# Performance work log

Measured on AMD Instinct MI355X. Metric: run time of the kernel, lower is better.

## Reference

```python
import jax, jax.numpy as jnp
import numpy as np

DIM = 768
HEADS = 6
HD = DIM // HEADS
B, N = 8, 4096
EPS = 1e-12  # torch F.normalize default


def setup_inputs() -> dict:
    key = jax.random.key(0)
    k1, k2, k3, k4, k5 = jax.random.split(key, 5)
    x = jax.random.normal(k1, (B, N, DIM), dtype=jnp.float32)
    y = jax.random.normal(k2, (B, N, DIM), dtype=jnp.float32)
    W_qkv = jax.random.normal(k3, (DIM, 2 * DIM), dtype=jnp.float32) * (1.0 / np.sqrt(DIM))
    temperature = jnp.ones((HEADS, 1, 1), dtype=jnp.float32)
    W_proj = jax.random.normal(k4, (DIM, DIM), dtype=jnp.float32) * (1.0 / np.sqrt(DIM))
    b_proj = jax.random.normal(k5, (DIM,), dtype=jnp.float32) * 0.01
    return {"x": x, "y": y, "W_qkv": W_qkv, "temperature": temperature,
            "W_proj": W_proj, "b_proj": b_proj}


def _l2norm(t):
    # F.normalize(dim=-1): v / max(||v||, eps)
    n = jnp.sqrt(jnp.sum(t * t, axis=-1, keepdims=True))
    return t / jnp.maximum(n, EPS)


def reference(x, y, W_qkv, temperature, W_proj, b_proj):
    Bx, Nx, C = x.shape
    # qkv: [B,N,2C] -> [B,N,2,H,hd] -> q,k: [B,H,hd,N]
    qkv = (x @ W_qkv).reshape(Bx, Nx, 2, HEADS, HD)
    qkv = jnp.transpose(qkv, (2, 0, 3, 4, 1))  # [2,B,H,hd,N]
    q, k = qkv[0], qkv[1]
    # v: [B,H,hd,N]
    v = jnp.transpose(y.reshape(Bx, Nx, HEADS, HD), (0, 2, 3, 1))
    q = _l2norm(q)  # normalize over token dim N
    k = _l2norm(k)
    # channel-channel attention: [B,H,hd,hd]
    attn = jnp.einsum('bhcn,bhdn->bhcd', q, k) * temperature
    attn = jax.nn.softmax(attn, axis=-1)
    out = jnp.einsum('bhcd,bhdn->bhcn', attn, v)  # [B,H,hd,N]
    out = jnp.transpose(out, (0, 3, 1, 2)).reshape(Bx, Nx, C)
    return out @ W_proj + b_proj
```

## Files before the change

### kernel.cpp

```cpp
#include <hip/hip_runtime.h>
#include <hip/hip_bf16.h>

using bf16 = __hip_bfloat16;
typedef __attribute__((ext_vector_type(4))) float f32x4;
typedef __attribute__((ext_vector_type(8))) short bf16x8;

constexpr int Ntok   = 4096;
constexpr int Cdim   = 768;
constexpr int Hn     = 6;
constexpr int HD     = 128;
constexpr int QKcols = 1536;
constexpr int NTRI   = 21;
constexpr int SPLITK = 4;

#define AS1 __attribute__((address_space(1)))
#define AS3 __attribute__((address_space(3)))

__device__ inline void gload_lds16(const bf16* g, bf16* l) {
    __builtin_amdgcn_global_load_lds((const AS1 void*)g, (AS3 void*)l, 16, 0, 0);
}

__device__ inline int4 cvt8_f32_to_bf16(const float* p) {
    const float4 a0 = *reinterpret_cast<const float4*>(p);
    const float4 a1 = *reinterpret_cast<const float4*>(p + 4);
    union { int4 i; bf16 h[8]; } u;
    u.h[0] = __float2bfloat16(a0.x); u.h[1] = __float2bfloat16(a0.y);
    u.h[2] = __float2bfloat16(a0.z); u.h[3] = __float2bfloat16(a0.w);
    u.h[4] = __float2bfloat16(a1.x); u.h[5] = __float2bfloat16(a1.y);
    u.h[6] = __float2bfloat16(a1.z); u.h[7] = __float2bfloat16(a1.w);
    return u.i;
}

__global__ __launch_bounds__(256) void cvt_kernel(const float* __restrict__ in,
                                                  bf16* __restrict__ out) {
    const size_t i = ((size_t)blockIdx.x * 256 + threadIdx.x) * 8;
    *reinterpret_cast<int4*>(out + i) = cvt8_f32_to_bf16(in + i);
}

__global__ void transpose_kernel(const float* __restrict__ W, bf16* __restrict__ Wt,
                                 int K, int N) {
    __shared__ bf16 tile[32][33];
    const int n0 = blockIdx.x * 32, k0 = blockIdx.y * 32;
    const int tx = threadIdx.x, ty = threadIdx.y;
    for (int i = 0; i < 32; i += 8)
        tile[ty + i][tx] = __float2bfloat16(W[(size_t)(k0 + ty + i) * N + n0 + tx]);
    __syncthreads();
    for (int i = 0; i < 32; i += 8)
        Wt[(size_t)(n0 + ty + i) * K + k0 + tx] = tile[tx][ty + i];
}

__global__ __launch_bounds__(256) void transpose_x(const float* __restrict__ x,
                                                   bf16* __restrict__ xT) {
    __shared__ bf16 tile[64][34];
    const int b = blockIdx.z, n0 = blockIdx.y * 64, c0 = blockIdx.x * 32;
    const int tid = threadIdx.x;
    const int c_r = tid & 31, n_r = tid >> 5;
    const float* xp = x + ((size_t)b * Ntok + n0) * Cdim + c0;
#pragma unroll
    for (int i = 0; i < 64; i += 8)
        tile[n_r + i][c_r] = __float2bfloat16(xp[(size_t)(n_r + i) * Cdim + c_r]);
    __syncthreads();
    const int n_w = tid & 63, c_w = tid >> 6;
    bf16* op = xT + ((size_t)b * Cdim + c0) * Ntok + n0;
#pragma unroll
    for (int i = 0; i < 32; i += 4)
        op[(size_t)(c_w + i) * Ntok + n_w] = tile[n_w][c_w + i];
}

template <bool C_F32, bool BIAS>
__global__ __launch_bounds__(256) void gemm_bt(const bf16* __restrict__ A,
                                               const bf16* __restrict__ Bt,
                                               const float* __restrict__ bias,
                                               void* __restrict__ Cv,
                                               int N, int K,
                                               size_t a_bs, size_t bt_bs, size_t c_bs) {
    __shared__ bf16 As[128 * 32];
    __shared__ bf16 Bs[128 * 32];

    A  += (size_t)blockIdx.z * a_bs;
    Bt += (size_t)blockIdx.z * bt_bs;
    const int m0   = blockIdx.y * 128, n0 = blockIdx.x * 128;
    const int tid  = threadIdx.x;
    const int wave = tid >> 6, lane = tid & 63;
    const int wq   = wave >> 1, wr = wave & 1;
    const int lm   = lane & 15, quad = lane >> 4;

    const int srow = tid >> 2, scol = (tid & 3) * 8;
    const bf16* Ag = A  + (size_t)(m0 + srow) * K + scol;
    const bf16* Bg = Bt + (size_t)(n0 + srow) * K + scol;
    bf16* Al0 = &As[srow * 32 + scol];
    bf16* Al1 = &As[(64 + srow) * 32 + scol];
    bf16* Bl0 = &Bs[srow * 32 + scol];
    bf16* Bl1 = &Bs[(64 + srow) * 32 + scol];

    f32x4 acc[4][4] = {};

    for (int k0 = 0; k0 < K; k0 += 32) {
        __syncthreads();
        gload_lds16(Ag + k0,                  Al0);
        gload_lds16(Ag + (size_t)64 * K + k0, Al1);
        gload_lds16(Bg + k0,                  Bl0);
        gload_lds16(Bg + (size_t)64 * K + k0, Bl1);
        __syncthreads();

        bf16x8 af[4], bfr[4];
#pragma unroll
        for (int t = 0; t < 4; t++) {
            af[t]  = *reinterpret_cast<const bf16x8*>(&As[(wq * 64 + t * 16 + lm) * 32 + quad * 8]);
            bfr[t] = *reinterpret_cast<const bf16x8*>(&Bs[(wr * 64 + t * 16 + lm) * 32 + quad * 8]);
        }
#pragma unroll
        for (int mt = 0; mt < 4; mt++)
#pragma unroll
            for (int nt = 0; nt < 4; nt++)
                acc[mt][nt] = __builtin_amdgcn_mfma_f32_16x16x32_bf16(af[mt], bfr[nt], acc[mt][nt], 0, 0, 0);
    }

    const int cm = m0 + wq * 64, cn = n0 + wr * 64;
#pragma unroll
    for (int mt = 0; mt < 4; mt++) {
#pragma unroll
        for (int nt = 0; nt < 4; nt++) {
            const int col = cn + nt * 16 + lm;
            const float bv = BIAS ? bias[col] : 0.0f;
#pragma unroll
            for (int r = 0; r < 4; r++) {
                const int row = cm + mt * 16 + quad * 4 + r;
                if constexpr (C_F32)
                    ((float*)Cv + (size_t)blockIdx.z * c_bs)[(size_t)row * N + col] = acc[mt][nt][r] + bv;
                else
                    ((bf16*)Cv + (size_t)blockIdx.z * c_bs)[(size_t)row * N + col] = __float2bfloat16(acc[mt][nt][r] + bv);
            }
        }
    }
}

__global__ __launch_bounds__(256) void gram_k(const bf16* __restrict__ xT,
                                              float* __restrict__ partial) {
    __shared__ bf16 As[128 * 32];
    __shared__ bf16 Bs[128 * 32];

    int ci = 0, rem = blockIdx.x, rowlen = 6;
    while (rem >= rowlen) { rem -= rowlen; rowlen--; ci++; }
    const int di = ci + rem;
    const int b = blockIdx.y, s = blockIdx.z;
    const int c0 = ci * 128, d0 = di * 128;

    const int tid  = threadIdx.x;
    const int wave = tid >> 6, lane = tid & 63;
    const int wq   = wave >> 1, wr = wave & 1;
    const int lm   = lane & 15, quad = lane >> 4;

    const int srow = tid >> 2, scol = (tid & 3) * 8;
    const size_t base = (size_t)b * Cdim * Ntok + (size_t)s * (Ntok / SPLITK);
    const bf16* Ag = xT + base + (size_t)(c0 + srow) * Ntok + scol;
    const bf16* Bg = xT + base + (size_t)(d0 + srow) * Ntok + scol;
    bf16* Al0 = &As[srow * 32 + scol];
    bf16* Al1 = &As[(64 + srow) * 32 + scol];
    bf16* Bl0 = &Bs[srow * 32 + scol];
    bf16* Bl1 = &Bs[(64 + srow) * 32 + scol];

    f32x4 acc[4][4] = {};

    for (int k0 = 0; k0 < Ntok / SPLITK; k0 += 32) {
        __syncthreads();
        gload_lds16(Ag + k0,                     Al0);
        gload_lds16(Ag + (size_t)64 * Ntok + k0, Al1);
        gload_lds16(Bg + k0,                     Bl0);
        gload_lds16(Bg + (size_t)64 * Ntok + k0, Bl1);
        __syncthreads();

        bf16x8 af[4], bfr[4];
#pragma unroll
        for (int t = 0; t < 4; t++) {
            af[t]  = *reinterpret_cast<const bf16x8*>(&As[(wq * 64 + t * 16 + lm) * 32 + quad * 8]);
            bfr[t] = *reinterpret_cast<const bf16x8*>(&Bs[(wr * 64 + t * 16 + lm) * 32 + quad * 8]);
        }
#pragma unroll
        for (int mt = 0; mt < 4; mt++)
#pragma unroll
            for (int nt = 0; nt < 4; nt++)
                acc[mt][nt] = __builtin_amdgcn_mfma_f32_16x16x32_bf16(af[mt], bfr[nt], acc[mt][nt], 0, 0, 0);
    }

    float* pp = partial + (((size_t)blockIdx.x * 8 + b) * SPLITK + s) * 16384;
#pragma unroll
    for (int mt = 0; mt < 4; mt++)
#pragma unroll
        for (int nt = 0; nt < 4; nt++)
#pragma unroll
            for (int r = 0; r < 4; r++)
                pp[(size_t)(wq * 64 + mt * 16 + quad * 4 + r) * 128 + wr * 64 + nt * 16 + lm] = acc[mt][nt][r];
}

__global__ __launch_bounds__(256) void gram_reduce(const float* __restrict__ partial,
                                                   bf16* __restrict__ G) {
    int ci = 0, rem = blockIdx.x, rowlen = 6;
    while (rem >= rowlen) { rem -= rowlen; rowlen--; ci++; }
    const int di = ci + rem, b = blockIdx.y;
    const int c0 = ci * 128, d0 = di * 128;
    const float* p0 = partial + ((size_t)blockIdx.x * 8 + b) * SPLITK * 16384;
    bf16* Gb = G + (size_t)b * Cdim * Cdim;
    const int tid = threadIdx.x;

    for (int i = 0; i < 16; i++) {
        const int off = i * 1024 + tid * 4;
        float4 v = *reinterpret_cast<const float4*>(p0 + off);
#pragma unroll
        for (int s2 = 1; s2 < SPLITK; s2++) {
            const float4 u = *reinterpret_cast<const float4*>(p0 + (size_t)s2 * 16384 + off);
            v.x += u.x; v.y += u.y; v.z += u.z; v.w += u.w;
        }
        const int c = off >> 7, d = off & 127;
        union { uint2 u2; bf16 h[4]; } pk;
        pk.h[0] = __float2bfloat16(v.x); pk.h[1] = __float2bfloat16(v.y);
        pk.h[2] = __float2bfloat16(v.z); pk.h[3] = __float2bfloat16(v.w);
        *reinterpret_cast<uint2*>(&Gb[(size_t)(c0 + c) * Cdim + d0 + d]) = pk.u2;
        if (ci != di) {
#pragma unroll
            for (int jj = 0; jj < 4; jj++)
                Gb[(size_t)(d0 + d + jj) * Cdim + c0 + c] = pk.h[jj];
        }
    }
}

__global__ __launch_bounds__(256) void diag_kernel(const bf16* __restrict__ Wtq,
                                                   const bf16* __restrict__ GWT,
                                                   float* __restrict__ invn) {
    const int b = blockIdx.y;
    const int col = blockIdx.x * 32 + (threadIdx.x >> 3);
    const int sub = threadIdx.x & 7;
    const bf16* w = Wtq + (size_t)col * Cdim + sub * 8;
    const bf16* g = GWT + ((size_t)b * QKcols + col) * Cdim + sub * 8;
    float s = 0.0f;
    for (int i = 0; i < 12; i++) {
        bf16 wv[8], gv[8];
        *reinterpret_cast<int4*>(wv) = *reinterpret_cast<const int4*>(w + i * 64);
        *reinterpret_cast<int4*>(gv) = *reinterpret_cast<const int4*>(g + i * 64);
#pragma unroll
        for (int u = 0; u < 8; u++) s += (float)wv[u] * (float)gv[u];
    }
    s += __shfl_xor(s, 1, 64);
    s += __shfl_xor(s, 2, 64);
    s += __shfl_xor(s, 4, 64);
    if (sub == 0)
        invn[(size_t)b * QKcols + col] = 1.0f / fmaxf(sqrtf(fmaxf(s, 0.0f)), 1e-12f);
}

__global__ __launch_bounds__(256) void head_kernel(const bf16* __restrict__ GWT,
                                                   const bf16* __restrict__ Wtq,
                                                   const float* __restrict__ invn,
                                                   const float* __restrict__ temp,
                                                   bf16* __restrict__ attnT) {
    constexpr int LDP = 136;
    __shared__ bf16 At[HD * LDP];

    const int bh = blockIdx.x, b = bh / Hn, h = bh % Hn;
    const int tid = threadIdx.x, wave = tid >> 6, lane = tid & 63;
    const int lm = lane & 15, quad = lane >> 4;
    const int qoff = h * HD, koff = Cdim + h * HD;
    const float th = temp[h];
    const float* invq = invn + (size_t)b * QKcols + qoff;
    const float* invk = invn + (size_t)b * QKcols + koff;

    f32x4 acc[2][8] = {};
    const bf16* Aq = Wtq + (size_t)(qoff + wave * 32 + lm) * Cdim + quad * 8;
    const bf16* Bk = GWT + ((size_t)b * QKcols + koff + lm) * Cdim + quad * 8;
    for (int r0 = 0; r0 < Cdim; r0 += 32) {
        bf16x8 aq[2], bk[8];
#pragma unroll
        for (int mt = 0; mt < 2; mt++)
            aq[mt] = *reinterpret_cast<const bf16x8*>(Aq + (size_t)mt * 16 * Cdim + r0);
#pragma unroll
        for (int dt = 0; dt < 8; dt++)
            bk[dt] = *reinterpret_cast<const bf16x8*>(Bk + (size_t)dt * 16 * Cdim + r0);
#pragma unroll
        for (int mt = 0; mt < 2; mt++)
#pragma unroll
            for (int dt = 0; dt < 8; dt++)
                acc[mt][dt] = __builtin_amdgcn_mfma_f32_16x16x32_bf16(aq[mt], bk[dt], acc[mt][dt], 0, 0, 0);
    }

    float ikv[8];
#pragma unroll
    for (int dt = 0; dt < 8; dt++) ikv[dt] = invk[dt * 16 + lm] * th;
#pragma unroll
    for (int mt = 0; mt < 2; mt++) {
#pragma unroll
        for (int r = 0; r < 4; r++) {
            const int c = wave * 32 + mt * 16 + quad * 4 + r;
            const float iq = invq[c];
            float v[8], m = -1e30f;
#pragma unroll
            for (int dt = 0; dt < 8; dt++) { v[dt] = acc[mt][dt][r] * iq * ikv[dt]; m = fmaxf(m, v[dt]); }
            m = fmaxf(m, __shfl_xor(m, 1, 64));
            m = fmaxf(m, __shfl_xor(m, 2, 64));
            m = fmaxf(m, __shfl_xor(m, 4, 64));
            m = fmaxf(m, __shfl_xor(m, 8, 64));
            float sum = 0.0f;
#pragma unroll
            for (int dt = 0; dt < 8; dt++) { v[dt] = __expf(v[dt] - m); sum += v[dt]; }
            sum += __shfl_xor(sum, 1, 64);
            sum += __shfl_xor(sum, 2, 64);
            sum += __shfl_xor(sum, 4, 64);
            sum += __shfl_xor(sum, 8, 64);
            const float inv = 1.0f / sum;
#pragma unroll
            for (int dt = 0; dt < 8; dt++)
                At[(dt * 16 + lm) * LDP + c] = __float2bfloat16(v[dt] * inv);
        }
    }
    __syncthreads();

#pragma unroll
    for (int i = 0; i < 8; i++) {
        const int idx = tid + 256 * i;
        const int d = idx >> 4, c8 = (idx & 15) * 8;
        const bf16x8 v = *reinterpret_cast<const bf16x8*>(&At[d * LDP + c8]);
        *reinterpret_cast<bf16x8*>(&attnT[((size_t)bh * HD + d) * HD + c8]) = v;
    }
}

__global__ __launch_bounds__(256) void fold_kernel(const bf16* __restrict__ attnT,
                                                   const bf16* __restrict__ Wtp,
                                                   bf16* __restrict__ WeffT) {
    const int j0 = blockIdx.x * 128, bh = blockIdx.y, b = bh / Hn, h = bh % Hn;
    const int tid = threadIdx.x, wave = tid >> 6, lane = tid & 63;
    const int lm = lane & 15, quad = lane >> 4;

    f32x4 acc[2][8] = {};
    const bf16* Ap = Wtp + (size_t)(j0 + wave * 32 + lm) * Cdim + h * HD + quad * 8;
    const bf16* Bd = attnT + ((size_t)bh * HD + lm) * HD + quad * 8;
#pragma unroll
    for (int ks = 0; ks < HD; ks += 32) {
        bf16x8 aw[2], bd[8];
#pragma unroll
        for (int mt = 0; mt < 2; mt++)
            aw[mt] = *reinterpret_cast<const bf16x8*>(Ap + (size_t)mt * 16 * Cdim + ks);
#pragma unroll
        for (int dt = 0; dt < 8; dt++)
            bd[dt] = *reinterpret_cast<const bf16x8*>(Bd + (size_t)dt * 16 * HD + ks);
#pragma unroll
        for (int mt = 0; mt < 2; mt++)
#pragma unroll
            for (int dt = 0; dt < 8; dt++)
                acc[mt][dt] = __builtin_amdgcn_mfma_f32_16x16x32_bf16(aw[mt], bd[dt], acc[mt][dt], 0, 0, 0);
    }

    bf16* Wo = WeffT + (size_t)b * Cdim * Cdim + h * HD;
#pragma unroll
    for (int mt = 0; mt < 2; mt++)
#pragma unroll
        for (int dt = 0; dt < 8; dt++)
#pragma unroll
            for (int r = 0; r < 4; r++)
                Wo[(size_t)(j0 + wave * 32 + mt * 16 + quad * 4 + r) * Cdim + dt * 16 + lm] =
                    __float2bfloat16(acc[mt][dt][r]);
}

extern "C" void kernel_launch(void* const* d_in, const int* in_sizes, int n_in,
                              void* d_out, int out_size, void* d_ws, size_t ws_size,
                              hipStream_t stream) {
    const float* x     = (const float*)d_in[0];
    const float* y     = (const float*)d_in[1];
    const float* Wqkv  = (const float*)d_in[2];
    const float* temp  = (const float*)d_in[3];
    const float* Wproj = (const float*)d_in[4];
    const float* bproj = (const float*)d_in[5];
    float* out = (float*)d_out;

    char* ws = (char*)d_ws;
    size_t o = 0;
    bf16*  xT      = (bf16*)(ws + o); o += (size_t)8 * Cdim * Ntok * 2;
    bf16*  yb      = (bf16*)(ws + o); o += (size_t)8 * Ntok * Cdim * 2;
    float* partial = (float*)(ws + o); o += (size_t)NTRI * 8 * SPLITK * 16384 * 4;
    bf16*  G       = (bf16*)(ws + o); o += (size_t)8 * Cdim * Cdim * 2;
    bf16*  GWT     = (bf16*)(ws + o); o += (size_t)8 * QKcols * Cdim * 2;
    bf16*  WeffT   = (bf16*)(ws + o); o += (size_t)8 * Cdim * Cdim * 2;
    bf16*  Wt_qkv  = (bf16*)(ws + o); o += (size_t)QKcols * Cdim * 2;
    bf16*  Wt_proj = (bf16*)(ws + o); o += (size_t)Cdim * Cdim * 2;
    float* invn    = (float*)(ws + o); o += (size_t)8 * QKcols * 4;
    bf16*  attnT   = (bf16*)(ws + o); o += (size_t)48 * HD * HD * 2;

    dim3 tb(32, 8);
    transpose_kernel<<<dim3(QKcols / 32, Cdim / 32), tb, 0, stream>>>(Wqkv, Wt_qkv, Cdim, QKcols);
    transpose_kernel<<<dim3(Cdim / 32, Cdim / 32), tb, 0, stream>>>(Wproj, Wt_proj, Cdim, Cdim);

    transpose_x<<<dim3(Cdim / 32, Ntok / 64, 8), 256, 0, stream>>>(x, xT);
    cvt_kernel<<<12288, 256, 0, stream>>>(y, yb);

    gram_k<<<dim3(NTRI, 8, SPLITK), 256, 0, stream>>>(xT, partial);
    gram_reduce<<<dim3(NTRI, 8), 256, 0, stream>>>(partial, G);

    gemm_bt<false, false><<<dim3(Cdim / 128, QKcols / 128, 8), 256, 0, stream>>>(
        Wt_qkv, G, nullptr, GWT, Cdim, Cdim,
        0, (size_t)Cdim * Cdim, (size_t)QKcols * Cdim);

    diag_kernel<<<dim3(QKcols / 32, 8), 256, 0, stream>>>(Wt_qkv, GWT, invn);
    head_kernel<<<48, 256, 0, stream>>>(GWT, Wt_qkv, invn, temp, attnT);
    fold_kernel<<<dim3(Cdim / 128, 48), 256, 0, stream>>>(attnT, Wt_proj, WeffT);

    gemm_bt<true, true><<<dim3(Cdim / 128, Ntok / 128, 8), 256, 0, stream>>>(
        yb, WeffT, bproj, out, Cdim, Cdim,
        (size_t)Ntok * Cdim, (size_t)Cdim * Cdim, (size_t)Ntok * Cdim);
}
```

Measured before the change: 489.4 us.

## Fuse transposes, head/diag/fold stages, and y conversion into final GEMM

Merges the x/W transposes into one launch, folds the diag norm computation and the projection fold into the per-head kernel, and converts fp32 y to bf16 inside the final GEMM's tile load instead of a separate pass. This removes the intermediate bf16 y buffer and several launches plus intermediate global writes. The final GEMM's A tiles now go through registers instead of async global-to-LDS loads. The fold work now runs on only 48 blocks, so it gets far less parallelism.

Result: faster. 460.3 us (-5.9%).

```diff
diff --git a/kernel.cpp b/kernel.cpp
--- a/kernel.cpp
+++ b/kernel.cpp
@@ -31,47 +31,42 @@
     return u.i;
 }
 
-__global__ __launch_bounds__(256) void cvt_kernel(const float* __restrict__ in,
-                                                  bf16* __restrict__ out) {
-    const size_t i = ((size_t)blockIdx.x * 256 + threadIdx.x) * 8;
-    *reinterpret_cast<int4*>(out + i) = cvt8_f32_to_bf16(in + i);
-}
-
-__global__ void transpose_kernel(const float* __restrict__ W, bf16* __restrict__ Wt,
-                                 int K, int N) {
-    __shared__ bf16 tile[32][33];
-    const int n0 = blockIdx.x * 32, k0 = blockIdx.y * 32;
-    const int tx = threadIdx.x, ty = threadIdx.y;
-    for (int i = 0; i < 32; i += 8)
-        tile[ty + i][tx] = __float2bfloat16(W[(size_t)(k0 + ty + i) * N + n0 + tx]);
-    __syncthreads();
-    for (int i = 0; i < 32; i += 8)
-        Wt[(size_t)(n0 + ty + i) * K + k0 + tx] = tile[tx][ty + i];
-}
-
-__global__ __launch_bounds__(256) void transpose_x(const float* __restrict__ x,
-                                                   bf16* __restrict__ xT) {
+__global__ __launch_bounds__(256) void transpose_all(const float* __restrict__ x,   bf16* __restrict__ xT,
+                                                     const float* __restrict__ Wqkv, bf16* __restrict__ Wtq,
+                                                     const float* __restrict__ Wproj, bf16* __restrict__ Wtp) {
     __shared__ bf16 tile[64][34];
-    const int b = blockIdx.z, n0 = blockIdx.y * 64, c0 = blockIdx.x * 32;
+    const int id = blockIdx.x;
+    const float* src; bf16* dst; int R, C, r0, c0;
+    if (id < 12288) {
+        const int b = id / 1536, rem = id % 1536;
+        r0 = (rem & 63) * 64; c0 = (rem >> 6) * 32;
+        R = Ntok; C = Cdim;
+        src = x + (size_t)b * Ntok * Cdim; dst = xT + (size_t)b * Cdim * Ntok;
+    } else if (id < 12864) {
+        const int rem = id - 12288;
+        r0 = (rem % 12) * 64; c0 = (rem / 12) * 32;
+        R = Cdim; C = QKcols; src = Wqkv; dst = Wtq;
+    } else {
+        const int rem = id - 12864;
+        r0 = (rem % 12) * 64; c0 = (rem / 12) * 32;
+        R = Cdim; C = Cdim; src = Wproj; dst = Wtp;
+    }
     const int tid = threadIdx.x;
     const int c_r = tid & 31, n_r = tid >> 5;
-    const float* xp = x + ((size_t)b * Ntok + n0) * Cdim + c0;
+    const float* sp = src + (size_t)(r0 + n_r) * C + c0 + c_r;
 #pragma unroll
     for (int i = 0; i < 64; i += 8)
-        tile[n_r + i][c_r] = __float2bfloat16(xp[(size_t)(n_r + i) * Cdim + c_r]);
+        tile[n_r + i][c_r] = __float2bfloat16(sp[(size_t)i * C]);
     __syncthreads();
     const int n_w = tid & 63, c_w = tid >> 6;
-    bf16* op = xT + ((size_t)b * Cdim + c0) * Ntok + n0;
 #pragma unroll
     for (int i = 0; i < 32; i += 4)
-        op[(size_t)(c_w + i) * Ntok + n_w] = tile[n_w][c_w + i];
-}
-
-template <bool C_F32, bool BIAS>
+        dst[(size_t)(c0 + c_w + i) * R + r0 + n_w] = tile[n_w][c_w + i];
+}
+
 __global__ __launch_bounds__(256) void gemm_bt(const bf16* __restrict__ A,
                                                const bf16* __restrict__ Bt,
-                                               const float* __restrict__ bias,
-                                               void* __restrict__ Cv,
+                                               bf16* __restrict__ Cv,
                                                int N, int K,
                                                size_t a_bs, size_t bt_bs, size_t c_bs) {
     __shared__ bf16 As[128 * 32];
@@ -116,23 +111,17 @@
                 acc[mt][nt] = __builtin_amdgcn_mfma_f32_16x16x32_bf16(af[mt], bfr[nt], acc[mt][nt], 0, 0, 0);
     }
 
+    bf16* Cb = Cv + (size_t)blockIdx.z * c_bs;
     const int cm = m0 + wq * 64, cn = n0 + wr * 64;
 #pragma unroll
-    for (int mt = 0; mt < 4; mt++) {
+    for (int mt = 0; mt < 4; mt++)
 #pragma unroll
         for (int nt = 0; nt < 4; nt++) {
             const int col = cn + nt * 16 + lm;
-            const float bv = BIAS ? bias[col] : 0.0f;
-#pragma unroll
-            for (int r = 0; r < 4; r++) {
-                const int row = cm + mt * 16 + quad * 4 + r;
-                if constexpr (C_F32)
-                    ((float*)Cv + (size_t)blockIdx.z * c_bs)[(size_t)row * N + col] = acc[mt][nt][r] + bv;
-                else
-                    ((bf16*)Cv + (size_t)blockIdx.z * c_bs)[(size_t)row * N + col] = __float2bfloat16(acc[mt][nt][r] + bv);
-            }
-        }
-    }
+#pragma unroll
+            for (int r = 0; r < 4; r++)
+                Cb[(size_t)(cm + mt * 16 + quad * 4 + r) * N + col] = __float2bfloat16(acc[mt][nt][r]);
+        }
 }
 
 __global__ __launch_bounds__(256) void gram_k(const bf16* __restrict__ xT,
@@ -140,10 +129,12 @@
     __shared__ bf16 As[128 * 32];
     __shared__ bf16 Bs[128 * 32];
 
-    int ci = 0, rem = blockIdx.x, rowlen = 6;
-    while (rem >= rowlen) { rem -= rowlen; rowlen--; ci++; }
-    const int di = ci + rem;
-    const int b = blockIdx.y, s = blockIdx.z;
+    const int bid = blockIdx.x;
+    const int b = bid & 7, rem = bid >> 3;
+    const int t = rem % 21, s = rem / 21;
+    int ci = 0, trem = t, rowlen = 6;
+    while (trem >= rowlen) { trem -= rowlen; rowlen--; ci++; }
+    const int di = ci + trem;
     const int c0 = ci * 128, d0 = di * 128;
 
     const int tid  = threadIdx.x;
@@ -172,9 +163,9 @@
 
         bf16x8 af[4], bfr[4];
 #pragma unroll
-        for (int t = 0; t < 4; t++) {
-            af[t]  = *reinterpret_cast<const bf16x8*>(&As[(wq * 64 + t * 16 + lm) * 32 + quad * 8]);
-            bfr[t] = *reinterpret_cast<const bf16x8*>(&Bs[(wr * 64 + t * 16 + lm) * 32 + quad * 8]);
+        for (int u = 0; u < 4; u++) {
+            af[u]  = *reinterpret_cast<const bf16x8*>(&As[(wq * 64 + u * 16 + lm) * 32 + quad * 8]);
+            bfr[u] = *reinterpret_cast<const bf16x8*>(&Bs[(wr * 64 + u * 16 + lm) * 32 + quad * 8]);
         }
 #pragma unroll
         for (int mt = 0; mt < 4; mt++)
@@ -183,7 +174,7 @@
                 acc[mt][nt] = __builtin_amdgcn_mfma_f32_16x16x32_bf16(af[mt], bfr[nt], acc[mt][nt], 0, 0, 0);
     }
 
-    float* pp = partial + (((size_t)blockIdx.x * 8 + b) * SPLITK + s) * 16384;
+    float* pp = partial + (((size_t)t * 8 + b) * SPLITK + s) * 16384;
 #pragma unroll
     for (int mt = 0; mt < 4; mt++)
 #pragma unroll
@@ -224,44 +215,49 @@
     }
 }
 
-__global__ __launch_bounds__(256) void diag_kernel(const bf16* __restrict__ Wtq,
-                                                   const bf16* __restrict__ GWT,
-                                                   float* __restrict__ invn) {
-    const int b = blockIdx.y;
-    const int col = blockIdx.x * 32 + (threadIdx.x >> 3);
-    const int sub = threadIdx.x & 7;
-    const bf16* w = Wtq + (size_t)col * Cdim + sub * 8;
-    const bf16* g = GWT + ((size_t)b * QKcols + col) * Cdim + sub * 8;
-    float s = 0.0f;
-    for (int i = 0; i < 12; i++) {
-        bf16 wv[8], gv[8];
-        *reinterpret_cast<int4*>(wv) = *reinterpret_cast<const int4*>(w + i * 64);
-        *reinterpret_cast<int4*>(gv) = *reinterpret_cast<const int4*>(g + i * 64);
-#pragma unroll
-        for (int u = 0; u < 8; u++) s += (float)wv[u] * (float)gv[u];
-    }
-    s += __shfl_xor(s, 1, 64);
-    s += __shfl_xor(s, 2, 64);
-    s += __shfl_xor(s, 4, 64);
-    if (sub == 0)
-        invn[(size_t)b * QKcols + col] = 1.0f / fmaxf(sqrtf(fmaxf(s, 0.0f)), 1e-12f);
-}
-
-__global__ __launch_bounds__(256) void head_kernel(const bf16* __restrict__ GWT,
-                                                   const bf16* __restrict__ Wtq,
-                                                   const float* __restrict__ invn,
-                                                   const float* __restrict__ temp,
-                                                   bf16* __restrict__ attnT) {
+__global__ __launch_bounds__(256) void head_all(const bf16* __restrict__ GWT,
+                                                const bf16* __restrict__ Wtq,
+                                                const bf16* __restrict__ Wtp,
+                                                const float* __restrict__ temp,
+                                                bf16* __restrict__ WeffT) {
     constexpr int LDP = 136;
     __shared__ bf16 At[HD * LDP];
+    __shared__ float invq[HD], invk[HD];
 
     const int bh = blockIdx.x, b = bh / Hn, h = bh % Hn;
     const int tid = threadIdx.x, wave = tid >> 6, lane = tid & 63;
     const int lm = lane & 15, quad = lane >> 4;
     const int qoff = h * HD, koff = Cdim + h * HD;
     const float th = temp[h];
-    const float* invq = invn + (size_t)b * QKcols + qoff;
-    const float* invk = invn + (size_t)b * QKcols + koff;
+
+    {
+        const int coli = tid >> 3, sub = tid & 7;
+#pragma unroll
+        for (int pass = 0; pass < 8; pass++) {
+            const int cl = pass * 32 + coli;
+            const int isk = cl >> 7;
+            const int col = (isk ? koff : qoff) + (cl & 127);
+            const bf16* w = Wtq + (size_t)col * Cdim + sub * 8;
+            const bf16* g = GWT + ((size_t)b * QKcols + col) * Cdim + sub * 8;
+            float s = 0.0f;
+#pragma unroll
+            for (int i = 0; i < 12; i++) {
+                bf16 wv[8], gv[8];
+                *reinterpret_cast<int4*>(wv) = *reinterpret_cast<const int4*>(w + i * 64);
+                *reinterpret_cast<int4*>(gv) = *reinterpret_cast<const int4*>(g + i * 64);
+#pragma unroll
+                for (int u = 0; u < 8; u++) s += (float)wv[u] * (float)gv[u];
+            }
+            s += __shfl_xor(s, 1, 64);
+            s += __shfl_xor(s, 2, 64);
+            s += __shfl_xor(s, 4, 64);
+            if (sub == 0) {
+                float* dst = isk ? invk : invq;
+                dst[cl & 127] = 1.0f / fmaxf(sqrtf(fmaxf(s, 0.0f)), 1e-12f);
+            }
+        }
+    }
+    __syncthreads();
 
     f32x4 acc[2][8] = {};
     const bf16* Aq = Wtq + (size_t)(qoff + wave * 32 + lm) * Cdim + quad * 8;
@@ -312,50 +308,98 @@
     }
     __syncthreads();
 
-#pragma unroll
-    for (int i = 0; i < 8; i++) {
-        const int idx = tid + 256 * i;
-        const int d = idx >> 4, c8 = (idx & 15) * 8;
-        const bf16x8 v = *reinterpret_cast<const bf16x8*>(&At[d * LDP + c8]);
-        *reinterpret_cast<bf16x8*>(&attnT[((size_t)bh * HD + d) * HD + c8]) = v;
-    }
-}
-
-__global__ __launch_bounds__(256) void fold_kernel(const bf16* __restrict__ attnT,
-                                                   const bf16* __restrict__ Wtp,
-                                                   bf16* __restrict__ WeffT) {
-    const int j0 = blockIdx.x * 128, bh = blockIdx.y, b = bh / Hn, h = bh % Hn;
-    const int tid = threadIdx.x, wave = tid >> 6, lane = tid & 63;
-    const int lm = lane & 15, quad = lane >> 4;
-
-    f32x4 acc[2][8] = {};
-    const bf16* Ap = Wtp + (size_t)(j0 + wave * 32 + lm) * Cdim + h * HD + quad * 8;
-    const bf16* Bd = attnT + ((size_t)bh * HD + lm) * HD + quad * 8;
-#pragma unroll
-    for (int ks = 0; ks < HD; ks += 32) {
-        bf16x8 aw[2], bd[8];
-#pragma unroll
-        for (int mt = 0; mt < 2; mt++)
-            aw[mt] = *reinterpret_cast<const bf16x8*>(Ap + (size_t)mt * 16 * Cdim + ks);
-#pragma unroll
-        for (int dt = 0; dt < 8; dt++)
-            bd[dt] = *reinterpret_cast<const bf16x8*>(Bd + (size_t)dt * 16 * HD + ks);
-#pragma unroll
-        for (int mt = 0; mt < 2; mt++)
+    bf16* Wo = WeffT + (size_t)b * Cdim * Cdim + h * HD;
+    for (int jo = 0; jo < Cdim; jo += 256) {
+        const int jb = jo + wave * 64;
+        f32x4 a2[4][8] = {};
+#pragma unroll
+        for (int ks = 0; ks < 4; ks++) {
+            bf16x8 aw[4], bp[8];
+#pragma unroll
+            for (int mt = 0; mt < 4; mt++)
+                aw[mt] = *reinterpret_cast<const bf16x8*>(Wtp + (size_t)(jb + mt * 16 + lm) * Cdim + h * HD + ks * 32 + quad * 8);
 #pragma unroll
             for (int dt = 0; dt < 8; dt++)
-                acc[mt][dt] = __builtin_amdgcn_mfma_f32_16x16x32_bf16(aw[mt], bd[dt], acc[mt][dt], 0, 0, 0);
-    }
-
-    bf16* Wo = WeffT + (size_t)b * Cdim * Cdim + h * HD;
-#pragma unroll
-    for (int mt = 0; mt < 2; mt++)
-#pragma unroll
-        for (int dt = 0; dt < 8; dt++)
+                bp[dt] = *reinterpret_cast<const bf16x8*>(&At[(dt * 16 + lm) * LDP + ks * 32 + quad * 8]);
+#pragma unroll
+            for (int mt = 0; mt < 4; mt++)
+#pragma unroll
+                for (int dt = 0; dt < 8; dt++)
+                    a2[mt][dt] = __builtin_amdgcn_mfma_f32_16x16x32_bf16(aw[mt], bp[dt], a2[mt][dt], 0, 0, 0);
+        }
+#pragma unroll
+        for (int mt = 0; mt < 4; mt++)
+#pragma unroll
+            for (int dt = 0; dt < 8; dt++)
+#pragma unroll
+                for (int r = 0; r < 4; r++)
+                    Wo[(size_t)(jb + mt * 16 + quad * 4 + r) * Cdim + dt * 16 + lm] =
+                        __float2bfloat16(a2[mt][dt][r]);
+    }
+}
+
+__global__ __launch_bounds__(256) void gemm_yfused(const float* __restrict__ Y,
+                                                   const bf16* __restrict__ WeffT,
+                                                   const float* __restrict__ bias,
+                                                   float* __restrict__ out) {
+    __shared__ bf16 As[128 * 32];
+    __shared__ bf16 Bs[128 * 32];
+
+    const int bid = blockIdx.x;
+    const int z = bid & 7, rem = bid >> 3;
+    const int bx = rem % 6, by = rem / 6;
+    const int m0 = by * 128, n0 = bx * 128;
+
+    const int tid  = threadIdx.x;
+    const int wave = tid >> 6, lane = tid & 63;
+    const int wq   = wave >> 1, wr = wave & 1;
+    const int lm   = lane & 15, quad = lane >> 4;
+
+    const int srow = tid >> 2, scol = (tid & 3) * 8;
+    const float* Ag = Y + (size_t)z * Ntok * Cdim + (size_t)(m0 + srow) * Cdim + scol;
+    const bf16*  Bg = WeffT + (size_t)z * Cdim * Cdim + (size_t)(n0 + srow) * Cdim + scol;
+    bf16* Al0 = &As[srow * 32 + scol];
+    bf16* Al1 = &As[(64 + srow) * 32 + scol];
+    bf16* Bl0 = &Bs[srow * 32 + scol];
+    bf16* Bl1 = &Bs[(64 + srow) * 32 + scol];
+
+    f32x4 acc[4][4] = {};
+
+    for (int k0 = 0; k0 < Cdim; k0 += 32) {
+        __syncthreads();
+        gload_lds16(Bg + k0,                     Bl0);
+        gload_lds16(Bg + (size_t)64 * Cdim + k0, Bl1);
+        const int4 a0 = cvt8_f32_to_bf16(Ag + k0);
+        const int4 a1 = cvt8_f32_to_bf16(Ag + (size_t)64 * Cdim + k0);
+        *reinterpret_cast<int4*>(Al0) = a0;
+        *reinterpret_cast<int4*>(Al1) = a1;
+        __syncthreads();
+
+        bf16x8 af[4], bfr[4];
+#pragma unroll
+        for (int t = 0; t < 4; t++) {
+            af[t]  = *reinterpret_cast<const bf16x8*>(&As[(wq * 64 + t * 16 + lm) * 32 + quad * 8]);
+            bfr[t] = *reinterpret_cast<const bf16x8*>(&Bs[(wr * 64 + t * 16 + lm) * 32 + quad * 8]);
+        }
+#pragma unroll
+        for (int mt = 0; mt < 4; mt++)
+#pragma unroll
+            for (int nt = 0; nt < 4; nt++)
+                acc[mt][nt] = __builtin_amdgcn_mfma_f32_16x16x32_bf16(af[mt], bfr[nt], acc[mt][nt], 0, 0, 0);
+    }
+
+    float* Ob = out + (size_t)z * Ntok * Cdim;
+    const int cm = m0 + wq * 64, cn = n0 + wr * 64;
+#pragma unroll
+    for (int mt = 0; mt < 4; mt++)
+#pragma unroll
+        for (int nt = 0; nt < 4; nt++) {
+            const int col = cn + nt * 16 + lm;
+            const float bv = bias[col];
 #pragma unroll
             for (int r = 0; r < 4; r++)
-                Wo[(size_t)(j0 + wave * 32 + mt * 16 + quad * 4 + r) * Cdim + dt * 16 + lm] =
-                    __float2bfloat16(acc[mt][dt][r]);
+                Ob[(size_t)(cm + mt * 16 + quad * 4 + r) * Cdim + col] = acc[mt][nt][r] + bv;
+        }
 }
 
 extern "C" void kernel_launch(void* const* d_in, const int* in_sizes, int n_in,
@@ -372,35 +416,24 @@
     char* ws = (char*)d_ws;
     size_t o = 0;
     bf16*  xT      = (bf16*)(ws + o); o += (size_t)8 * Cdim * Ntok * 2;
-    bf16*  yb      = (bf16*)(ws + o); o += (size_t)8 * Ntok * Cdim * 2;
     float* partial = (float*)(ws + o); o += (size_t)NTRI * 8 * SPLITK * 16384 * 4;
     bf16*  G       = (bf16*)(ws + o); o += (size_t)8 * Cdim * Cdim * 2;
     bf16*  GWT     = (bf16*)(ws + o); o += (size_t)8 * QKcols * Cdim * 2;
     bf16*  WeffT   = (bf16*)(ws + o); o += (size_t)8 * Cdim * Cdim * 2;
     bf16*  Wt_qkv  = (bf16*)(ws + o); o += (size_t)QKcols * Cdim * 2;
     bf16*  Wt_proj = (bf16*)(ws + o); o += (size_t)Cdim * Cdim * 2;
-    float* invn    = (float*)(ws + o); o += (size_t)8 * QKcols * 4;
-    bf16*  attnT   = (bf16*)(ws + o); o += (size_t)48 * HD * HD * 2;
-
-    dim3 tb(32, 8);
-    transpose_kernel<<<dim3(QKcols / 32, Cdim / 32), tb, 0, stream>>>(Wqkv, Wt_qkv, Cdim, QKcols);
-    transpose_kernel<<<dim3(Cdim / 32, Cdim / 32), tb, 0, stream>>>(Wproj, Wt_proj, Cdim, Cdim);
-
-    transpose_x<<<dim3(Cdim / 32, Ntok / 64, 8), 256, 0, stream>>>(x, xT);
-    cvt_kernel<<<12288, 256, 0, stream>>>(y, yb);
-
-    gram_k<<<dim3(NTRI, 8, SPLITK), 256, 0, stream>>>(xT, partial);
+
+    transpose_all<<<13152, 256, 0, stream>>>(x, xT, Wqkv, Wt_qkv, Wproj, Wt_proj);
+
+    gram_k<<<NTRI * 8 * SPLITK, 256, 0, stream>>>(xT, partial);
+
     gram_reduce<<<dim3(NTRI, 8), 256, 0, stream>>>(partial, G);
 
-    gemm_bt<false, false><<<dim3(Cdim / 128, QKcols / 128, 8), 256, 0, stream>>>(
-        Wt_qkv, G, nullptr, GWT, Cdim, Cdim,
+    gemm_bt<<<dim3(Cdim / 128, QKcols / 128, 8), 256, 0, stream>>>(
+        Wt_qkv, G, GWT, Cdim, Cdim,
         0, (size_t)Cdim * Cdim, (size_t)QKcols * Cdim);
 
-    diag_kernel<<<dim3(QKcols / 32, 8), 256, 0, stream>>>(Wt_qkv, GWT, invn);
-    head_kernel<<<48, 256, 0, stream>>>(GWT, Wt_qkv, invn, temp, attnT);
-    fold_kernel<<<dim3(Cdim / 128, 48), 256, 0, stream>>>(attnT, Wt_proj, WeffT);
-
-    gemm_bt<true, true><<<dim3(Cdim / 128, Ntok / 128, 8), 256, 0, stream>>>(
-        yb, WeffT, bproj, out, Cdim, Cdim,
-        (size_t)Ntok * Cdim, (size_t)Cdim * Cdim, (size_t)Ntok * Cdim);
-}
+    head_all<<<48, 256, 0, stream>>>(GWT, Wt_qkv, Wt_proj, temp, WeffT);
+
+    gemm_yfused<<<1536, 256, 0, stream>>>(y, WeffT, bproj, out);
+}
```
